# Kernel optimization log

Hardware: AMD Instinct MI355X
Metric: run time of the kernel (lower is better)

## Reference

```python
import jax, jax.numpy as jnp
import numpy as np

DIM = 1024
NUM_HEADS = 16
HEAD_DIM = DIM // NUM_HEADS
SCALE = HEAD_DIM ** -0.5


def setup_inputs() -> dict:
    key = jax.random.key(0)
    ks = jax.random.split(key, 6)
    B, N, C = 2, 2048, DIM
    std = C ** -0.5
    return {
        "x_t": jax.random.normal(ks[0], (B, N, C), dtype=jnp.float32),
        "x_s": jax.random.normal(ks[1], (B, N, C), dtype=jnp.float32),
        "W_q": jax.random.normal(ks[2], (C, C), dtype=jnp.float32) * std,
        "W_kv": jax.random.normal(ks[3], (C, 2 * C), dtype=jnp.float32) * std,
        "W_fuse": jax.random.normal(ks[4], (C, C), dtype=jnp.float32) * std,
        "b_fuse": jax.random.normal(ks[5], (C,), dtype=jnp.float32) * 0.01,
    }


def reference(x_t, x_s, W_q, W_kv, W_fuse, b_fuse):
    B, N, C = x_t.shape
    H, D = NUM_HEADS, HEAD_DIM
    # q projection (no bias, qkv_bias=False): [B,N,C] -> [B,H,N,D]
    q = (x_t @ W_q).reshape(B, N, H, D).transpose(0, 2, 1, 3)
    # kv projection: [B,N,2C] -> k,v each [B,H,N,D]
    kv = (x_s @ W_kv).reshape(B, N, 2, H, D).transpose(2, 0, 3, 1, 4)
    k, v = kv[0], kv[1]
    # attention scores [B,H,N,N]
    attn = jnp.einsum("bhnd,bhmd->bhnm", q, k) * SCALE
    attn = jax.nn.softmax(attn, axis=-1)
    # weighted values -> [B,N,C]
    a = jnp.einsum("bhnm,bhmd->bhnd", attn, v).transpose(0, 2, 1, 3).reshape(B, N, C)
    # fuse projection (with bias); dropouts are identity (p=0)
    return a @ W_fuse + b_fuse
```

## Files before the change

### kernel.cpp

```cpp
#include <hip/hip_runtime.h>

#define SEQ 2048

typedef short short8 __attribute__((ext_vector_type(8)));
typedef float floatx4 __attribute__((ext_vector_type(4)));

static __device__ __forceinline__ unsigned short f2bf(float f) {
    unsigned int u = __builtin_bit_cast(unsigned int, f);
    u = (u + 0x7fffu + ((u >> 16) & 1u)) >> 16;
    return (unsigned short)u;
}

#define GLD16(gp, lp)                                                        \
    __builtin_amdgcn_global_load_lds(                                        \
        (const __attribute__((address_space(1))) unsigned int*)(gp),         \
        (__attribute__((address_space(3))) unsigned int*)(lp), 16, 0, 0)

__global__ void cvt2_kernel(const float4* __restrict__ a, const float4* __restrict__ b,
                            ushort4* __restrict__ oa, ushort4* __restrict__ ob, float sa) {
    int i = blockIdx.x * blockDim.x + threadIdx.x;
    if (i < 1048576) {
        float4 v = a[i];
        ushort4 o;
        o.x = f2bf(v.x * sa); o.y = f2bf(v.y * sa);
        o.z = f2bf(v.z * sa); o.w = f2bf(v.w * sa);
        oa[i] = o;
    } else {
        int j = i - 1048576;
        float4 v = b[j];
        ushort4 o;
        o.x = f2bf(v.x); o.y = f2bf(v.y);
        o.z = f2bf(v.z); o.w = f2bf(v.w);
        ob[j] = o;
    }
}

__global__ void transpose_all(const float* __restrict__ Wq, const float* __restrict__ Wkv,
                              const float* __restrict__ Wf,
                              unsigned short* __restrict__ oq, unsigned short* __restrict__ okv,
                              unsigned short* __restrict__ of_) {
    __shared__ float tile[32][33];
    int bx = blockIdx.x;
    const float* in; unsigned short* out; int N, t;
    if (bx < 1024)      { in = Wq;  out = oq;  N = 1024; t = bx; }
    else if (bx < 3072) { in = Wkv; out = okv; N = 2048; t = bx - 1024; }
    else                { in = Wf;  out = of_; N = 1024; t = bx - 3072; }
    int nb = N >> 5;
    int n0 = (t % nb) * 32, k0 = (t / nb) * 32;
    int tx = threadIdx.x, ty = threadIdx.y;
#pragma unroll
    for (int i = 0; i < 4; i++)
        tile[ty + i * 8][tx] = in[(size_t)(k0 + ty + i * 8) * N + n0 + tx];
    __syncthreads();
#pragma unroll
    for (int i = 0; i < 4; i++)
        out[(size_t)(n0 + ty + i * 8) * 1024 + k0 + tx] = f2bf(tile[tx][ty + i * 8]);
}

__global__ __launch_bounds__(256, 3)
void gemm_qkv(const unsigned short* __restrict__ xt,
              const unsigned short* __restrict__ xs,
              const unsigned short* __restrict__ wq,
              const unsigned short* __restrict__ wkv,
              unsigned short* __restrict__ q_ws,
              unsigned short* __restrict__ k_ws,
              unsigned short* __restrict__ vt_ws) {
    __shared__ unsigned short sA[128][64];
    __shared__ unsigned short sB[128][64];
    int tid = threadIdx.x, wave = tid >> 6, lane = tid & 63;
    int l15 = lane & 15, quad = lane >> 4;
    int cx = blockIdx.x;
    bool isq = cx < 8;
    const unsigned short* A  = isq ? xt : xs;
    const unsigned short* Bt = isq ? wq : wkv;
    int C0 = (isq ? cx : cx - 8) * 128;
    int R0 = blockIdx.y * 128;
    int wr = (wave >> 1) * 64, wc = (wave & 1) * 64;
    int srow = lane >> 3, scol = (lane & 7) * 8;

    floatx4 acc[4][4];
#pragma unroll
    for (int i = 0; i < 4; i++)
#pragma unroll
        for (int j = 0; j < 4; j++) acc[i][j] = (floatx4){0.f, 0.f, 0.f, 0.f};

    for (int kt = 0; kt < 16; kt++) {
        __syncthreads();
#pragma unroll
        for (int c = 0; c < 4; c++) {
            int rb = wave * 32 + c * 8;
            GLD16(&A [(size_t)(R0 + rb + srow) * 1024 + kt * 64 + scol], &sA[rb][0]);
            GLD16(&Bt[(size_t)(C0 + rb + srow) * 1024 + kt * 64 + scol], &sB[rb][0]);
        }
        __syncthreads();
#pragma unroll
        for (int ks = 0; ks < 2; ks++) {
            short8 af[4], bf[4];
#pragma unroll
            for (int mt = 0; mt < 4; mt++)
                af[mt] = *(const short8*)&sA[wr + mt * 16 + l15][ks * 32 + quad * 8];
#pragma unroll
            for (int nt = 0; nt < 4; nt++)
                bf[nt] = *(const short8*)&sB[wc + nt * 16 + l15][ks * 32 + quad * 8];
#pragma unroll
            for (int mt = 0; mt < 4; mt++)
#pragma unroll
                for (int nt = 0; nt < 4; nt++)
                    acc[mt][nt] = __builtin_amdgcn_mfma_f32_16x16x32_bf16(af[mt], bf[nt], acc[mt][nt], 0, 0, 0);
        }
    }

    int b = R0 >> 11, nb0 = (R0 & 2047) + wr;
#pragma unroll
    for (int mt = 0; mt < 4; mt++) {
#pragma unroll
        for (int nt = 0; nt < 4; nt++) {
            int col = C0 + wc + nt * 16 + l15;
            if (isq) {
                int h = col >> 6, d = col & 63;
#pragma unroll
                for (int r = 0; r < 4; r++) {
                    int n = nb0 + mt * 16 + quad * 4 + r;
                    q_ws[((size_t)((b * 16 + h) * 2048 + n)) * 64 + d] = f2bf(acc[mt][nt][r]);
                }
            } else if (col < 1024) {
                int h = col >> 6, d = col & 63;
#pragma unroll
                for (int r = 0; r < 4; r++) {
                    int n = nb0 + mt * 16 + quad * 4 + r;
                    k_ws[((size_t)((b * 16 + h) * 2048 + n)) * 64 + d] = f2bf(acc[mt][nt][r]);
                }
            } else {
                int cc = col - 1024, h = cc >> 6, d = cc & 63;
                int n = nb0 + mt * 16 + quad * 4;
                ushort4 pk;
                pk.x = f2bf(acc[mt][nt][0]); pk.y = f2bf(acc[mt][nt][1]);
                pk.z = f2bf(acc[mt][nt][2]); pk.w = f2bf(acc[mt][nt][3]);
                *(ushort4*)&vt_ws[((size_t)((b * 16 + h) * 64 + d)) * 2048 + n] = pk;
            }
        }
    }
}

__global__ __launch_bounds__(256, 3)
void gemm_fuse(const unsigned short* __restrict__ A,
               const unsigned short* __restrict__ Bt,
               float* __restrict__ out, const float* __restrict__ bias) {
    __shared__ unsigned short sA[128][64];
    __shared__ unsigned short sB[64][64];
    int tid = threadIdx.x, wave = tid >> 6, lane = tid & 63;
    int l15 = lane & 15, quad = lane >> 4;
    int R0 = blockIdx.y * 128, C0 = blockIdx.x * 64;
    int wr = (wave >> 1) * 64, wc = (wave & 1) * 32;
    int srow = lane >> 3, scol = (lane & 7) * 8;

    floatx4 acc[4][2];
#pragma unroll
    for (int i = 0; i < 4; i++)
#pragma unroll
        for (int j = 0; j < 2; j++) acc[i][j] = (floatx4){0.f, 0.f, 0.f, 0.f};

    for (int kt = 0; kt < 16; kt++) {
        __syncthreads();
#pragma unroll
        for (int c = 0; c < 4; c++) {
            int rb = wave * 32 + c * 8;
            GLD16(&A[(size_t)(R0 + rb + srow) * 1024 + kt * 64 + scol], &sA[rb][0]);
        }
#pragma unroll
        for (int c = 0; c < 2; c++) {
            int rb = wave * 16 + c * 8;
            GLD16(&Bt[(size_t)(C0 + rb + srow) * 1024 + kt * 64 + scol], &sB[rb][0]);
        }
        __syncthreads();
#pragma unroll
        for (int ks = 0; ks < 2; ks++) {
            short8 af[4], bf[2];
#pragma unroll
            for (int mt = 0; mt < 4; mt++)
                af[mt] = *(const short8*)&sA[wr + mt * 16 + l15][ks * 32 + quad * 8];
#pragma unroll
            for (int nt = 0; nt < 2; nt++)
                bf[nt] = *(const short8*)&sB[wc + nt * 16 + l15][ks * 32 + quad * 8];
#pragma unroll
            for (int mt = 0; mt < 4; mt++)
#pragma unroll
                for (int nt = 0; nt < 2; nt++)
                    acc[mt][nt] = __builtin_amdgcn_mfma_f32_16x16x32_bf16(af[mt], bf[nt], acc[mt][nt], 0, 0, 0);
        }
    }

#pragma unroll
    for (int mt = 0; mt < 4; mt++) {
#pragma unroll
        for (int r = 0; r < 4; r++) {
            int row = R0 + wr + mt * 16 + quad * 4 + r;
#pragma unroll
            for (int nt = 0; nt < 2; nt++) {
                int col = C0 + wc + nt * 16 + l15;
                out[(size_t)row * 1024 + col] = acc[mt][nt][r] + bias[col];
            }
        }
    }
}

__global__ __launch_bounds__(256, 2)
void attn_kernel(const unsigned short* __restrict__ Q,
                 const unsigned short* __restrict__ K,
                 const unsigned short* __restrict__ Vt,
                 unsigned short* __restrict__ Aout) {
    __shared__ unsigned short sQ[128][72];
    __shared__ unsigned short sK[2][64][72];
    __shared__ unsigned short sV[2][64][72];
    __shared__ unsigned short sP[4][32][72];

    int tid = threadIdx.x, wave = tid >> 6, lane = tid & 63;
    int l15 = lane & 15, quad = lane >> 4;
    int bh = blockIdx.y, b = bh >> 4, h = bh & 15;
    int qr0 = blockIdx.x * 128;

    const unsigned short* Qp = Q + (size_t)bh * SEQ * 64;
    const unsigned short* Kp = K + (size_t)bh * SEQ * 64;
    const unsigned short* Vp = Vt + (size_t)bh * 64 * SEQ;

#pragma unroll
    for (int i = 0; i < 4; i++) {
        int ch = tid + i * 256;
        int row = ch >> 3, kc = (ch & 7) * 8;
        *(int4*)&sQ[row][kc] = *(const int4*)&Qp[(size_t)(qr0 + row) * 64 + kc];
    }
#pragma unroll
    for (int i = 0; i < 2; i++) {
        int ch = tid + i * 256;
        int row = ch >> 3, kc = (ch & 7) * 8;
        *(int4*)&sK[0][row][kc] = *(const int4*)&Kp[(size_t)row * 64 + kc];
        *(int4*)&sV[0][row][kc] = *(const int4*)&Vp[(size_t)row * SEQ + kc];
    }
    __syncthreads();

    short8 qf[2][2];
#pragma unroll
    for (int qt = 0; qt < 2; qt++)
#pragma unroll
        for (int ks = 0; ks < 2; ks++)
            qf[qt][ks] = *(const short8*)&sQ[wave * 32 + qt * 16 + l15][ks * 32 + quad * 8];

    floatx4 of[4][2];
#pragma unroll
    for (int i = 0; i < 4; i++)
#pragma unroll
        for (int j = 0; j < 2; j++) of[i][j] = (floatx4){0.f, 0.f, 0.f, 0.f};
    floatx4 lacc[2] = {(floatx4){0.f, 0.f, 0.f, 0.f}, (floatx4){0.f, 0.f, 0.f, 0.f}};

    for (int kt = 0; kt < 32; kt++) {
        int p = kt & 1;
        int4 kreg[2], vreg[2];
        if (kt < 31) {
            int k0n = (kt + 1) * 64;
#pragma unroll
            for (int i = 0; i < 2; i++) {
                int ch = tid + i * 256;
                int row = ch >> 3, kc = (ch & 7) * 8;
                kreg[i] = *(const int4*)&Kp[(size_t)(k0n + row) * 64 + kc];
                vreg[i] = *(const int4*)&Vp[(size_t)row * SEQ + k0n + kc];
            }
        }

        floatx4 sacc[4][2];
        floatx4 zero = (floatx4){0.f, 0.f, 0.f, 0.f};
#pragma unroll
        for (int f = 0; f < 4; f++) {
            short8 kf0 = *(const short8*)&sK[p][f * 16 + l15][quad * 8];
            short8 kf1 = *(const short8*)&sK[p][f * 16 + l15][32 + quad * 8];
#pragma unroll
            for (int qt = 0; qt < 2; qt++) {
                floatx4 t = __builtin_amdgcn_mfma_f32_16x16x32_bf16(kf0, qf[qt][0], zero, 0, 0, 0);
                sacc[f][qt] = __builtin_amdgcn_mfma_f32_16x16x32_bf16(kf1, qf[qt][1], t, 0, 0, 0);
            }
        }

#pragma unroll
        for (int qt = 0; qt < 2; qt++) {
#pragma unroll
            for (int f = 0; f < 4; f++) {
                floatx4 pv;
#pragma unroll
                for (int r = 0; r < 4; r++)
                    pv[r] = __builtin_amdgcn_exp2f(sacc[f][qt][r]);
                lacc[qt] += pv;
                ushort4 pk;
                pk.x = f2bf(pv[0]); pk.y = f2bf(pv[1]);
                pk.z = f2bf(pv[2]); pk.w = f2bf(pv[3]);
                *(ushort4*)&sP[wave][qt * 16 + l15][f * 16 + quad * 4] = pk;
            }
        }
        asm volatile("s_waitcnt lgkmcnt(0)" ::: "memory");

#pragma unroll
        for (int s2 = 0; s2 < 2; s2++) {
            short8 pf[2];
#pragma unroll
            for (int qt = 0; qt < 2; qt++)
                pf[qt] = *(const short8*)&sP[wave][qt * 16 + l15][s2 * 32 + quad * 8];
#pragma unroll
            for (int dt = 0; dt < 4; dt++) {
                short8 vf = *(const short8*)&sV[p][dt * 16 + l15][s2 * 32 + quad * 8];
#pragma unroll
                for (int qt = 0; qt < 2; qt++)
                    of[dt][qt] = __builtin_amdgcn_mfma_f32_16x16x32_bf16(vf, pf[qt], of[dt][qt], 0, 0, 0);
            }
        }

        if (kt < 31) {
#pragma unroll
            for (int i = 0; i < 2; i++) {
                int ch = tid + i * 256;
                int row = ch >> 3, kc = (ch & 7) * 8;
                *(int4*)&sK[p ^ 1][row][kc] = kreg[i];
                *(int4*)&sV[p ^ 1][row][kc] = vreg[i];
            }
            __syncthreads();
        }
    }

    float l_fin[2];
#pragma unroll
    for (int qt = 0; qt < 2; qt++) {
        float s = lacc[qt][0] + lacc[qt][1] + lacc[qt][2] + lacc[qt][3];
        s += __shfl_xor(s, 16, 64);
        s += __shfl_xor(s, 32, 64);
        l_fin[qt] = s;
    }

#pragma unroll
    for (int qt = 0; qt < 2; qt++) {
        float inv = 1.f / l_fin[qt];
        int row = qr0 + wave * 32 + qt * 16 + l15;
        size_t base = (size_t)(b * SEQ + row) * 1024 + h * 64;
#pragma unroll
        for (int dt = 0; dt < 4; dt++) {
            ushort4 o;
            o.x = f2bf(of[dt][qt][0] * inv);
            o.y = f2bf(of[dt][qt][1] * inv);
            o.z = f2bf(of[dt][qt][2] * inv);
            o.w = f2bf(of[dt][qt][3] * inv);
            *(ushort4*)&Aout[base + dt * 16 + quad * 4] = o;
        }
    }
}

extern "C" void kernel_launch(void* const* d_in, const int* in_sizes, int n_in,
                              void* d_out, int out_size, void* d_ws, size_t ws_size,
                              hipStream_t stream) {
    const float* x_t  = (const float*)d_in[0];
    const float* x_s  = (const float*)d_in[1];
    const float* W_q  = (const float*)d_in[2];
    const float* W_kv = (const float*)d_in[3];
    const float* W_f  = (const float*)d_in[4];
    const float* b_f  = (const float*)d_in[5];
    float* out = (float*)d_out;

    char* ws = (char*)d_ws;
    const size_t MB = 1u << 20;
    unsigned short* xt_bf = (unsigned short*)(ws);
    unsigned short* xs_bf = (unsigned short*)(ws + 8 * MB);
    unsigned short* wq_t  = (unsigned short*)(ws + 16 * MB);
    unsigned short* wkv_t = (unsigned short*)(ws + 18 * MB);
    unsigned short* wf_t  = (unsigned short*)(ws + 22 * MB);
    unsigned short* q_ws  = (unsigned short*)(ws + 24 * MB);
    unsigned short* k_ws  = (unsigned short*)(ws + 32 * MB);
    unsigned short* vt_ws = (unsigned short*)(ws + 40 * MB);
    unsigned short* a_ws  = (unsigned short*)(ws + 48 * MB);

    cvt2_kernel<<<8192, 256, 0, stream>>>((const float4*)x_t, (const float4*)x_s,
                                          (ushort4*)xt_bf, (ushort4*)xs_bf,
                                          0.125f * 1.44269504088896340736f);
    transpose_all<<<4096, dim3(32, 8), 0, stream>>>(W_q, W_kv, W_f, wq_t, wkv_t, wf_t);

    gemm_qkv<<<dim3(24, 32), 256, 0, stream>>>(xt_bf, xs_bf, wq_t, wkv_t, q_ws, k_ws, vt_ws);
    attn_kernel<<<dim3(16, 32), 256, 0, stream>>>(q_ws, k_ws, vt_ws, a_ws);
    gemm_fuse<<<dim3(16, 32), 256, 0, stream>>>(a_ws, wf_t, out, b_f);
}
```

Baseline: 210.3 us.

## Reuse Q shared buffer for P, shrink LDS padding, raise attention occupancy

```diff
diff --git a/kernel.cpp b/kernel.cpp
--- a/kernel.cpp
+++ b/kernel.cpp
@@ -10,6 +10,18 @@
     u = (u + 0x7fffu + ((u >> 16) & 1u)) >> 16;
     return (unsigned short)u;
 }
+
+#if __has_builtin(__builtin_amdgcn_cvt_pk_bf16_f32)
+typedef __bf16 bf16x2 __attribute__((ext_vector_type(2)));
+static __device__ __forceinline__ unsigned int pk_bf16(float a, float b) {
+    bf16x2 v = __builtin_amdgcn_cvt_pk_bf16_f32(a, b);
+    return __builtin_bit_cast(unsigned int, v);
+}
+#else
+static __device__ __forceinline__ unsigned int pk_bf16(float a, float b) {
+    return (unsigned int)f2bf(a) | ((unsigned int)f2bf(b) << 16);
+}
+#endif
 
 #define GLD16(gp, lp)                                                        \
     __builtin_amdgcn_global_load_lds(                                        \
@@ -204,15 +216,14 @@
     }
 }
 
-__global__ __launch_bounds__(256, 2)
+__global__ __launch_bounds__(256, 3)
 void attn_kernel(const unsigned short* __restrict__ Q,
                  const unsigned short* __restrict__ K,
                  const unsigned short* __restrict__ Vt,
                  unsigned short* __restrict__ Aout) {
-    __shared__ unsigned short sQ[128][72];
-    __shared__ unsigned short sK[2][64][72];
-    __shared__ unsigned short sV[2][64][72];
-    __shared__ unsigned short sP[4][32][72];
+    __shared__ unsigned short sQ[128][68];
+    __shared__ unsigned short sK[2][64][68];
+    __shared__ unsigned short sV[2][64][68];
 
     int tid = threadIdx.x, wave = tid >> 6, lane = tid & 63;
     int l15 = lane & 15, quad = lane >> 4;
@@ -244,6 +255,9 @@
 #pragma unroll
         for (int ks = 0; ks < 2; ks++)
             qf[qt][ks] = *(const short8*)&sQ[wave * 32 + qt * 16 + l15][ks * 32 + quad * 8];
+    __syncthreads();
+
+    unsigned short (*sP)[68] = (unsigned short (*)[68])(&sQ[wave * 32][0]);
 
     floatx4 of[4][2];
 #pragma unroll
@@ -288,10 +302,10 @@
                 for (int r = 0; r < 4; r++)
                     pv[r] = __builtin_amdgcn_exp2f(sacc[f][qt][r]);
                 lacc[qt] += pv;
-                ushort4 pk;
-                pk.x = f2bf(pv[0]); pk.y = f2bf(pv[1]);
-                pk.z = f2bf(pv[2]); pk.w = f2bf(pv[3]);
-                *(ushort4*)&sP[wave][qt * 16 + l15][f * 16 + quad * 4] = pk;
+                uint2 pk;
+                pk.x = pk_bf16(pv[0], pv[1]);
+                pk.y = pk_bf16(pv[2], pv[3]);
+                *(uint2*)&sP[qt * 16 + l15][f * 16 + quad * 4] = pk;
             }
         }
         asm volatile("s_waitcnt lgkmcnt(0)" ::: "memory");
@@ -301,7 +315,7 @@
             short8 pf[2];
 #pragma unroll
             for (int qt = 0; qt < 2; qt++)
-                pf[qt] = *(const short8*)&sP[wave][qt * 16 + l15][s2 * 32 + quad * 8];
+                pf[qt] = *(const short8*)&sP[qt * 16 + l15][s2 * 32 + quad * 8];
 #pragma unroll
             for (int dt = 0; dt < 4; dt++) {
                 short8 vf = *(const short8*)&sV[p][dt * 16 + l15][s2 * 32 + quad * 8];
@@ -339,12 +353,10 @@
         size_t base = (size_t)(b * SEQ + row) * 1024 + h * 64;
 #pragma unroll
         for (int dt = 0; dt < 4; dt++) {
-            ushort4 o;
-            o.x = f2bf(of[dt][qt][0] * inv);
-            o.y = f2bf(of[dt][qt][1] * inv);
-            o.z = f2bf(of[dt][qt][2] * inv);
-            o.w = f2bf(of[dt][qt][3] * inv);
-            *(ushort4*)&Aout[base + dt * 16 + quad * 4] = o;
+            uint2 o;
+            o.x = pk_bf16(of[dt][qt][0] * inv, of[dt][qt][1] * inv);
+            o.y = pk_bf16(of[dt][qt][2] * inv, of[dt][qt][3] * inv);
+            *(uint2*)&Aout[base + dt * 16 + quad * 4] = o;
         }
     }
 }
```

Result: slower. 233.2 us (+10.9%).

## Double-buffer LDS tiles in projection GEMMs to overlap loads with MFMA

Applied to the files above, without the earlier changes.

```diff
diff --git a/kernel.cpp b/kernel.cpp
--- a/kernel.cpp
+++ b/kernel.cpp
@@ -57,7 +57,7 @@
         out[(size_t)(n0 + ty + i * 8) * 1024 + k0 + tx] = f2bf(tile[tx][ty + i * 8]);
 }
 
-__global__ __launch_bounds__(256, 3)
+__global__ __launch_bounds__(256, 2)
 void gemm_qkv(const unsigned short* __restrict__ xt,
               const unsigned short* __restrict__ xs,
               const unsigned short* __restrict__ wq,
@@ -65,8 +65,8 @@
               unsigned short* __restrict__ q_ws,
               unsigned short* __restrict__ k_ws,
               unsigned short* __restrict__ vt_ws) {
-    __shared__ unsigned short sA[128][64];
-    __shared__ unsigned short sB[128][64];
+    __shared__ unsigned short sA[2][128][64];
+    __shared__ unsigned short sB[2][128][64];
     int tid = threadIdx.x, wave = tid >> 6, lane = tid & 63;
     int l15 = lane & 15, quad = lane >> 4;
     int cx = blockIdx.x;
@@ -84,30 +84,42 @@
 #pragma unroll
         for (int j = 0; j < 4; j++) acc[i][j] = (floatx4){0.f, 0.f, 0.f, 0.f};
 
+#pragma unroll
+    for (int c = 0; c < 4; c++) {
+        int rb = wave * 32 + c * 8;
+        GLD16(&A [(size_t)(R0 + rb + srow) * 1024 + scol], &sA[0][rb][0]);
+        GLD16(&Bt[(size_t)(C0 + rb + srow) * 1024 + scol], &sB[0][rb][0]);
+    }
+
     for (int kt = 0; kt < 16; kt++) {
-        __syncthreads();
-#pragma unroll
-        for (int c = 0; c < 4; c++) {
-            int rb = wave * 32 + c * 8;
-            GLD16(&A [(size_t)(R0 + rb + srow) * 1024 + kt * 64 + scol], &sA[rb][0]);
-            GLD16(&Bt[(size_t)(C0 + rb + srow) * 1024 + kt * 64 + scol], &sB[rb][0]);
-        }
-        __syncthreads();
+        int p = kt & 1;
+        if (kt < 15) {
+#pragma unroll
+            for (int c = 0; c < 4; c++) {
+                int rb = wave * 32 + c * 8;
+                GLD16(&A [(size_t)(R0 + rb + srow) * 1024 + (kt + 1) * 64 + scol], &sA[p ^ 1][rb][0]);
+                GLD16(&Bt[(size_t)(C0 + rb + srow) * 1024 + (kt + 1) * 64 + scol], &sB[p ^ 1][rb][0]);
+            }
+            asm volatile("s_waitcnt vmcnt(8)\n\ts_barrier" ::: "memory");
+        } else {
+            asm volatile("s_waitcnt vmcnt(0)\n\ts_barrier" ::: "memory");
+        }
 #pragma unroll
         for (int ks = 0; ks < 2; ks++) {
             short8 af[4], bf[4];
 #pragma unroll
             for (int mt = 0; mt < 4; mt++)
-                af[mt] = *(const short8*)&sA[wr + mt * 16 + l15][ks * 32 + quad * 8];
+                af[mt] = *(const short8*)&sA[p][wr + mt * 16 + l15][ks * 32 + quad * 8];
 #pragma unroll
             for (int nt = 0; nt < 4; nt++)
-                bf[nt] = *(const short8*)&sB[wc + nt * 16 + l15][ks * 32 + quad * 8];
+                bf[nt] = *(const short8*)&sB[p][wc + nt * 16 + l15][ks * 32 + quad * 8];
 #pragma unroll
             for (int mt = 0; mt < 4; mt++)
 #pragma unroll
                 for (int nt = 0; nt < 4; nt++)
                     acc[mt][nt] = __builtin_amdgcn_mfma_f32_16x16x32_bf16(af[mt], bf[nt], acc[mt][nt], 0, 0, 0);
         }
+        asm volatile("s_barrier" ::: "memory");
     }
 
     int b = R0 >> 11, nb0 = (R0 & 2047) + wr;
@@ -146,8 +158,8 @@
 void gemm_fuse(const unsigned short* __restrict__ A,
                const unsigned short* __restrict__ Bt,
                float* __restrict__ out, const float* __restrict__ bias) {
-    __shared__ unsigned short sA[128][64];
-    __shared__ unsigned short sB[64][64];
+    __shared__ unsigned short sA[2][128][64];
+    __shared__ unsigned short sB[2][64][64];
     int tid = threadIdx.x, wave = tid >> 6, lane = tid & 63;
     int l15 = lane & 15, quad = lane >> 4;
     int R0 = blockIdx.y * 128, C0 = blockIdx.x * 64;
@@ -160,34 +172,50 @@
 #pragma unroll
         for (int j = 0; j < 2; j++) acc[i][j] = (floatx4){0.f, 0.f, 0.f, 0.f};
 
+#pragma unroll
+    for (int c = 0; c < 4; c++) {
+        int rb = wave * 32 + c * 8;
+        GLD16(&A[(size_t)(R0 + rb + srow) * 1024 + scol], &sA[0][rb][0]);
+    }
+#pragma unroll
+    for (int c = 0; c < 2; c++) {
+        int rb = wave * 16 + c * 8;
+        GLD16(&Bt[(size_t)(C0 + rb + srow) * 1024 + scol], &sB[0][rb][0]);
+    }
+
     for (int kt = 0; kt < 16; kt++) {
-        __syncthreads();
-#pragma unroll
-        for (int c = 0; c < 4; c++) {
-            int rb = wave * 32 + c * 8;
-            GLD16(&A[(size_t)(R0 + rb + srow) * 1024 + kt * 64 + scol], &sA[rb][0]);
-        }
-#pragma unroll
-        for (int c = 0; c < 2; c++) {
-            int rb = wave * 16 + c * 8;
-            GLD16(&Bt[(size_t)(C0 + rb + srow) * 1024 + kt * 64 + scol], &sB[rb][0]);
-        }
-        __syncthreads();
+        int p = kt & 1;
+        if (kt < 15) {
+#pragma unroll
+            for (int c = 0; c < 4; c++) {
+                int rb = wave * 32 + c * 8;
+                GLD16(&A[(size_t)(R0 + rb + srow) * 1024 + (kt + 1) * 64 + scol], &sA[p ^ 1][rb][0]);
+            }
+#pragma unroll
+            for (int c = 0; c < 2; c++) {
+                int rb = wave * 16 + c * 8;
+                GLD16(&Bt[(size_t)(C0 + rb + srow) * 1024 + (kt + 1) * 64 + scol], &sB[p ^ 1][rb][0]);
+            }
+            asm volatile("s_waitcnt vmcnt(6)\n\ts_barrier" ::: "memory");
+        } else {
+            asm volatile("s_waitcnt vmcnt(0)\n\ts_barrier" ::: "memory");
+        }
 #pragma unroll
         for (int ks = 0; ks < 2; ks++) {
             short8 af[4], bf[2];
 #pragma unroll
             for (int mt = 0; mt < 4; mt++)
-                af[mt] = *(const short8*)&sA[wr + mt * 16 + l15][ks * 32 + quad * 8];
+                af[mt] = *(const short8*)&sA[p][wr + mt * 16 + l15][ks * 32 + quad * 8];
 #pragma unroll
             for (int nt = 0; nt < 2; nt++)
-                bf[nt] = *(const short8*)&sB[wc + nt * 16 + l15][ks * 32 + quad * 8];
+                bf[nt] = *(const short8*)&sB[p][wc + nt * 16 + l15][ks * 32 + quad * 8];
 #pragma unroll
             for (int mt = 0; mt < 4; mt++)
 #pragma unroll
                 for (int nt = 0; nt < 2; nt++)
                     acc[mt][nt] = __builtin_amdgcn_mfma_f32_16x16x32_bf16(af[mt], bf[nt], acc[mt][nt], 0, 0, 0);
         }
+        asm volatile("s_barrier" ::: "memory");
     }
 
 #pragma unroll
```

Result: slower. 220.3 us (+4.7%).

## Halve attention query tile, reuse Q smem for P, swizzle LDS

Applied to the files above, without the earlier changes.

```diff
diff --git a/kernel.cpp b/kernel.cpp
--- a/kernel.cpp
+++ b/kernel.cpp
@@ -15,6 +15,8 @@
     __builtin_amdgcn_global_load_lds(                                        \
         (const __attribute__((address_space(1))) unsigned int*)(gp),         \
         (__attribute__((address_space(3))) unsigned int*)(lp), 16, 0, 0)
+
+#define SWZ(row, col) ((col) ^ (((row) & 7) << 3))
 
 __global__ void cvt2_kernel(const float4* __restrict__ a, const float4* __restrict__ b,
                             ushort4* __restrict__ oa, ushort4* __restrict__ ob, float sa) {
@@ -204,53 +206,46 @@
     }
 }
 
-__global__ __launch_bounds__(256, 2)
+__global__ __launch_bounds__(256, 4)
 void attn_kernel(const unsigned short* __restrict__ Q,
                  const unsigned short* __restrict__ K,
                  const unsigned short* __restrict__ Vt,
                  unsigned short* __restrict__ Aout) {
-    __shared__ unsigned short sQ[128][72];
-    __shared__ unsigned short sK[2][64][72];
-    __shared__ unsigned short sV[2][64][72];
-    __shared__ unsigned short sP[4][32][72];
+    __shared__ unsigned short sQP[64][64];
+    __shared__ unsigned short sK[2][64][64];
+    __shared__ unsigned short sV[2][64][64];
 
     int tid = threadIdx.x, wave = tid >> 6, lane = tid & 63;
     int l15 = lane & 15, quad = lane >> 4;
     int bh = blockIdx.y, b = bh >> 4, h = bh & 15;
-    int qr0 = blockIdx.x * 128;
+    int qr0 = blockIdx.x * 64;
 
     const unsigned short* Qp = Q + (size_t)bh * SEQ * 64;
     const unsigned short* Kp = K + (size_t)bh * SEQ * 64;
     const unsigned short* Vp = Vt + (size_t)bh * 64 * SEQ;
 
 #pragma unroll
-    for (int i = 0; i < 4; i++) {
-        int ch = tid + i * 256;
-        int row = ch >> 3, kc = (ch & 7) * 8;
-        *(int4*)&sQ[row][kc] = *(const int4*)&Qp[(size_t)(qr0 + row) * 64 + kc];
-    }
-#pragma unroll
     for (int i = 0; i < 2; i++) {
         int ch = tid + i * 256;
         int row = ch >> 3, kc = (ch & 7) * 8;
-        *(int4*)&sK[0][row][kc] = *(const int4*)&Kp[(size_t)row * 64 + kc];
-        *(int4*)&sV[0][row][kc] = *(const int4*)&Vp[(size_t)row * SEQ + kc];
+        *(int4*)&sQP[row][SWZ(row, kc)] = *(const int4*)&Qp[(size_t)(qr0 + row) * 64 + kc];
+        *(int4*)&sK[0][row][SWZ(row, kc)] = *(const int4*)&Kp[(size_t)row * 64 + kc];
+        *(int4*)&sV[0][row][SWZ(row, kc)] = *(const int4*)&Vp[(size_t)row * SEQ + kc];
     }
     __syncthreads();
 
-    short8 qf[2][2];
-#pragma unroll
-    for (int qt = 0; qt < 2; qt++)
-#pragma unroll
-        for (int ks = 0; ks < 2; ks++)
-            qf[qt][ks] = *(const short8*)&sQ[wave * 32 + qt * 16 + l15][ks * 32 + quad * 8];
-
-    floatx4 of[4][2];
-#pragma unroll
-    for (int i = 0; i < 4; i++)
-#pragma unroll
-        for (int j = 0; j < 2; j++) of[i][j] = (floatx4){0.f, 0.f, 0.f, 0.f};
-    floatx4 lacc[2] = {(floatx4){0.f, 0.f, 0.f, 0.f}, (floatx4){0.f, 0.f, 0.f, 0.f}};
+    short8 qf[2];
+#pragma unroll
+    for (int ks = 0; ks < 2; ks++) {
+        int row = wave * 16 + l15;
+        qf[ks] = *(const short8*)&sQP[row][SWZ(row, ks * 32 + quad * 8)];
+    }
+    __syncthreads();
+
+    floatx4 of[4];
+#pragma unroll
+    for (int i = 0; i < 4; i++) of[i] = (floatx4){0.f, 0.f, 0.f, 0.f};
+    floatx4 lacc = (floatx4){0.f, 0.f, 0.f, 0.f};
 
     for (int kt = 0; kt < 32; kt++) {
         int p = kt & 1;
@@ -266,48 +261,41 @@
             }
         }
 
-        floatx4 sacc[4][2];
+        floatx4 sacc[4];
         floatx4 zero = (floatx4){0.f, 0.f, 0.f, 0.f};
 #pragma unroll
         for (int f = 0; f < 4; f++) {
-            short8 kf0 = *(const short8*)&sK[p][f * 16 + l15][quad * 8];
-            short8 kf1 = *(const short8*)&sK[p][f * 16 + l15][32 + quad * 8];
-#pragma unroll
-            for (int qt = 0; qt < 2; qt++) {
-                floatx4 t = __builtin_amdgcn_mfma_f32_16x16x32_bf16(kf0, qf[qt][0], zero, 0, 0, 0);
-                sacc[f][qt] = __builtin_amdgcn_mfma_f32_16x16x32_bf16(kf1, qf[qt][1], t, 0, 0, 0);
-            }
-        }
-
-#pragma unroll
-        for (int qt = 0; qt < 2; qt++) {
-#pragma unroll
-            for (int f = 0; f < 4; f++) {
-                floatx4 pv;
-#pragma unroll
-                for (int r = 0; r < 4; r++)
-                    pv[r] = __builtin_amdgcn_exp2f(sacc[f][qt][r]);
-                lacc[qt] += pv;
-                ushort4 pk;
-                pk.x = f2bf(pv[0]); pk.y = f2bf(pv[1]);
-                pk.z = f2bf(pv[2]); pk.w = f2bf(pv[3]);
-                *(ushort4*)&sP[wave][qt * 16 + l15][f * 16 + quad * 4] = pk;
-            }
+            int krow = f * 16 + l15;
+            short8 kf0 = *(const short8*)&sK[p][krow][SWZ(krow, quad * 8)];
+            short8 kf1 = *(const short8*)&sK[p][krow][SWZ(krow, 32 + quad * 8)];
+            floatx4 t = __builtin_amdgcn_mfma_f32_16x16x32_bf16(kf0, qf[0], zero, 0, 0, 0);
+            sacc[f] = __builtin_amdgcn_mfma_f32_16x16x32_bf16(kf1, qf[1], t, 0, 0, 0);
+        }
+
+#pragma unroll
+        for (int f = 0; f < 4; f++) {
+            floatx4 pv;
+#pragma unroll
+            for (int r = 0; r < 4; r++)
+                pv[r] = __builtin_amdgcn_exp2f(sacc[f][r]);
+            lacc += pv;
+            ushort4 pk;
+            pk.x = f2bf(pv[0]); pk.y = f2bf(pv[1]);
+            pk.z = f2bf(pv[2]); pk.w = f2bf(pv[3]);
+            int prow = wave * 16 + l15;
+            *(ushort4*)&sQP[prow][SWZ(prow, f * 16 + quad * 4)] = pk;
         }
         asm volatile("s_waitcnt lgkmcnt(0)" ::: "memory");
 
 #pragma unroll
         for (int s2 = 0; s2 < 2; s2++) {
-            short8 pf[2];
-#pragma unroll
-            for (int qt = 0; qt < 2; qt++)
-                pf[qt] = *(const short8*)&sP[wave][qt * 16 + l15][s2 * 32 + quad * 8];
+            int prow = wave * 16 + l15;
+            short8 pf = *(const short8*)&sQP[prow][SWZ(prow, s2 * 32 + quad * 8)];
 #pragma unroll
             for (int dt = 0; dt < 4; dt++) {
-                short8 vf = *(const short8*)&sV[p][dt * 16 + l15][s2 * 32 + quad * 8];
-#pragma unroll
-                for (int qt = 0; qt < 2; qt++)
-                    of[dt][qt] = __builtin_amdgcn_mfma_f32_16x16x32_bf16(vf, pf[qt], of[dt][qt], 0, 0, 0);
+                int vrow = dt * 16 + l15;
+                short8 vf = *(const short8*)&sV[p][vrow][SWZ(vrow, s2 * 32 + quad * 8)];
+                of[dt] = __builtin_amdgcn_mfma_f32_16x16x32_bf16(vf, pf, of[dt], 0, 0, 0);
             }
         }
 
@@ -316,34 +304,32 @@
             for (int i = 0; i < 2; i++) {
                 int ch = tid + i * 256;
                 int row = ch >> 3, kc = (ch & 7) * 8;
-                *(int4*)&sK[p ^ 1][row][kc] = kreg[i];
-                *(int4*)&sV[p ^ 1][row][kc] = vreg[i];
+                *(int4*)&sK[p ^ 1][row][SWZ(row, kc)] = kreg[i];
+                *(int4*)&sV[p ^ 1][row][SWZ(row, kc)] = vreg[i];
             }
             __syncthreads();
         }
     }
 
-    float l_fin[2];
-#pragma unroll
-    for (int qt = 0; qt < 2; qt++) {
-        float s = lacc[qt][0] + lacc[qt][1] + lacc[qt][2] + lacc[qt][3];
+    float l_fin;
+    {
+        float s = lacc[0] + lacc[1] + lacc[2] + lacc[3];
         s += __shfl_xor(s, 16, 64);
         s += __shfl_xor(s, 32, 64);
-        l_fin[qt] = s;
-    }
-
-#pragma unroll
-    for (int qt = 0; qt < 2; qt++) {
-        float inv = 1.f / l_fin[qt];
-        int row = qr0 + wave * 32 + qt * 16 + l15;
+        l_fin = s;
+    }
+
+    {
+        float inv = 1.f / l_fin;
+        int row = qr0 + wave * 16 + l15;
         size_t base = (size_t)(b * SEQ + row) * 1024 + h * 64;
 #pragma unroll
         for (int dt = 0; dt < 4; dt++) {
             ushort4 o;
-            o.x = f2bf(of[dt][qt][0] * inv);
-            o.y = f2bf(of[dt][qt][1] * inv);
-            o.z = f2bf(of[dt][qt][2] * inv);
-            o.w = f2bf(of[dt][qt][3] * inv);
+            o.x = f2bf(of[dt][0] * inv);
+            o.y = f2bf(of[dt][1] * inv);
+            o.z = f2bf(of[dt][2] * inv);
+            o.w = f2bf(of[dt][3] * inv);
             *(ushort4*)&Aout[base + dt * 16 + quad * 4] = o;
         }
     }
@@ -378,6 +364,6 @@
     transpose_all<<<4096, dim3(32, 8), 0, stream>>>(W_q, W_kv, W_f, wq_t, wkv_t, wf_t);
 
     gemm_qkv<<<dim3(24, 32), 256, 0, stream>>>(xt_bf, xs_bf, wq_t, wkv_t, q_ws, k_ws, vt_ws);
-    attn_kernel<<<dim3(16, 32), 256, 0, stream>>>(q_ws, k_ws, vt_ws, a_ws);
+    attn_kernel<<<dim3(32, 32), 256, 0, stream>>>(q_ws, k_ws, vt_ws, a_ws);
     gemm_fuse<<<dim3(16, 32), 256, 0, stream>>>(a_ws, wf_t, out, b_f);
 }
```

Measured after the change: 215.9 us. 2.6% more time.
